# Optimization experiments

Hardware: AMD Instinct MI355X
Metric: run time of the kernel (lower is better)

Reference implementation:

```python
import jax, jax.numpy as jnp
import numpy as np
from jax import lax


def setup_inputs() -> dict:
    key = jax.random.key(0)
    k1, k2, k3, k4 = jax.random.split(key, 4)
    B, D, L = 2, 4096, 4096
    G, HL = 256, 128
    x = jax.random.normal(k1, (B, D, L), dtype=jnp.float32)
    k = jax.random.normal(k2, (B, D, L), dtype=jnp.float32)
    q = jax.random.normal(k3, (B, D, L), dtype=jnp.float32)
    h = jax.random.normal(k4, (G, HL), dtype=jnp.float32)
    return {"x": x, "k": k, "q": q, "h": h}


def reference(x, k, q, h):
    # Hyena-SE gated causal long conv (unfused_gcg reference path, bdl layout):
    #   kx = k * x ; y = causal_depthwise_conv(kx, h) ; out = q * y
    B, D, L = x.shape
    G, HL = h.shape
    # torch ref: h.squeeze(1).repeat(d // num_groups, 1)  -> tile filters over channels
    w = jnp.tile(h, (D // G, 1))[:, None, :]  # (D, 1, HL)
    kx = k * x
    y = lax.conv_general_dilated(
        kx, w,
        window_strides=(1,),
        padding=[(HL - 1, 0)],  # causal left pad
        dimension_numbers=("NCH", "OIH", "NCH"),
        feature_group_count=D,
    )  # (B, D, L)
    return q * y
```

## Files before the change

kernel.cpp:

```cpp
#include <hip/hip_runtime.h>


#define HSE_B  2
#define HSE_D  4096
#define HSE_L  4096
#define HSE_G  256
#define HSE_HL 128

constexpr int TPB  = 256;
constexpr int VPT  = 16;
constexpr int PAD  = 128;
constexpr int BUFN = PAD + HSE_L;
constexpr int ROWS = 4;
constexpr int GRID = (HSE_B * HSE_D) / ROWS;

__device__ __forceinline__ int swiz(int i) {
    return i ^ (((i >> 5) & 7) << 2);
}

__global__ __launch_bounds__(TPB, 4) void hyena_se_kernel(
    const float* __restrict__ x, const float* __restrict__ k,
    const float* __restrict__ q, const float* __restrict__ h,
    float* __restrict__ out)
{
    __shared__ float skx[2 * BUFN];

    const int tid  = threadIdx.x;
    const int t0   = tid * VPT;
    const int row0 = blockIdx.x * ROWS;

    if (tid < PAD / 4) {
        float4 z = make_float4(0.f, 0.f, 0.f, 0.f);
        ((float4*)skx)[swiz(4 * tid) >> 2] = z;
        ((float4*)(skx + BUFN))[swiz(4 * tid) >> 2] = z;
    }

    {
        const size_t row = (size_t)row0 * HSE_L;
        #pragma unroll
        for (int r = 0; r < HSE_L / (4 * TPB); ++r) {
            int pos = 4 * (tid + TPB * r);
            float4 xv = *(const float4*)(x + row + pos);
            float4 kv = *(const float4*)(k + row + pos);
            ((float4*)skx)[swiz(PAD + pos) >> 2] =
                make_float4(xv.x * kv.x, xv.y * kv.y, xv.z * kv.z, xv.w * kv.w);
        }
    }
    __syncthreads();

    for (int rr = 0; rr < ROWS; ++rr) {
        const int cur = rr & 1;
        float* __restrict__ buf = skx + cur * BUFN;
        const size_t row = (size_t)(row0 + rr) * HSE_L;
        const int d = (row0 + rr) & (HSE_D - 1);
        const float* __restrict__ hrow = h + (size_t)(d & (HSE_G - 1)) * HSE_HL;

        float4 qv[VPT / 4];
        #pragma unroll
        for (int m = 0; m < VPT / 4; ++m)
            qv[m] = *(const float4*)(q + row + t0 + 4 * m);

        float4 xn[4], kn[4];
        const bool more = (rr + 1 < ROWS);
        if (more) {
            const size_t nrow = row + HSE_L;
            #pragma unroll
            for (int r = 0; r < 4; ++r) {
                int pos = 4 * (tid + TPB * r);
                xn[r] = *(const float4*)(x + nrow + pos);
                kn[r] = *(const float4*)(k + nrow + pos);
            }
        }

        float acc[VPT];
        #pragma unroll
        for (int v = 0; v < VPT; ++v) acc[v] = 0.f;

        float w[24];
        #pragma unroll
        for (int m = 0; m < 4; ++m) {
            float4 wv = ((const float4*)buf)[swiz(t0 + 4 * m) >> 2];
            w[4*m+0] = wv.x; w[4*m+1] = wv.y; w[4*m+2] = wv.z; w[4*m+3] = wv.w;
        }

        #pragma unroll
        for (int jc = 0; jc < HSE_HL / 8; ++jc) {
            #pragma unroll
            for (int m = 0; m < 2; ++m) {
                float4 wv = ((const float4*)buf)[swiz(t0 + 8 * jc + 16 + 4 * m) >> 2];
                w[16 + 4*m + 0] = wv.x; w[16 + 4*m + 1] = wv.y;
                w[16 + 4*m + 2] = wv.z; w[16 + 4*m + 3] = wv.w;
            }
            float hf[8];
            #pragma unroll
            for (int u = 0; u < 8; ++u) hf[u] = hrow[8 * jc + u];

            #pragma unroll
            for (int v = 0; v < VPT; ++v) {
                #pragma unroll
                for (int u = 0; u < 8; ++u) {
                    acc[v] = fmaf(hf[u], w[1 + v + u], acc[v]);
                }
            }
            #pragma unroll
            for (int p = 0; p < 16; ++p) w[p] = w[p + 8];
        }

        #pragma unroll
        for (int m = 0; m < VPT / 4; ++m) {
            float4 o;
            o.x = qv[m].x * acc[4*m + 0];
            o.y = qv[m].y * acc[4*m + 1];
            o.z = qv[m].z * acc[4*m + 2];
            o.w = qv[m].w * acc[4*m + 3];
            *(float4*)(out + row + t0 + 4 * m) = o;
        }

        if (more) {
            float* __restrict__ nbuf = skx + (cur ^ 1) * BUFN;
            #pragma unroll
            for (int r = 0; r < 4; ++r) {
                int pos = 4 * (tid + TPB * r);
                ((float4*)nbuf)[swiz(PAD + pos) >> 2] = make_float4(
                    xn[r].x * kn[r].x, xn[r].y * kn[r].y,
                    xn[r].z * kn[r].z, xn[r].w * kn[r].w);
            }
        }
        __syncthreads();
    }
}

extern "C" void kernel_launch(void* const* d_in, const int* in_sizes, int n_in,
                              void* d_out, int out_size, void* d_ws, size_t ws_size,
                              hipStream_t stream) {
    const float* x = (const float*)d_in[0];
    const float* k = (const float*)d_in[1];
    const float* q = (const float*)d_in[2];
    const float* h = (const float*)d_in[3];
    float* o = (float*)d_out;

    dim3 grid(GRID);
    dim3 block(TPB);
    hyena_se_kernel<<<grid, block, 0, stream>>>(x, k, q, h, o);
}
```

Before: 460.9 us.

## Prefetch x/k via async global-to-LDS loads and use a persistent-style grid

```diff
diff --git a/kernel.cpp b/kernel.cpp
--- a/kernel.cpp
+++ b/kernel.cpp
@@ -10,67 +10,87 @@
 constexpr int TPB  = 256;
 constexpr int VPT  = 16;
 constexpr int PAD  = 128;
-constexpr int BUFN = PAD + HSE_L;
-constexpr int ROWS = 4;
-constexpr int GRID = (HSE_B * HSE_D) / ROWS;
+constexpr int LDS_KX = PAD + HSE_L;
+constexpr int GRID = 768;
+constexpr int BASE_ROWS = (HSE_B * HSE_D) / GRID;
 
 __device__ __forceinline__ int swiz(int i) {
     return i ^ (((i >> 5) & 7) << 2);
 }
 
-__global__ __launch_bounds__(TPB, 4) void hyena_se_kernel(
+__device__ __forceinline__ void gload16(const float* gp, float* lp) {
+    __builtin_amdgcn_global_load_lds(
+        (const __attribute__((address_space(1))) void*)gp,
+        (__attribute__((address_space(3))) void*)lp,
+        16, 0, 0);
+}
+
+__global__ __launch_bounds__(TPB, 3) void hyena_se_kernel(
     const float* __restrict__ x, const float* __restrict__ k,
     const float* __restrict__ q, const float* __restrict__ h,
     float* __restrict__ out)
 {
-    __shared__ float skx[2 * BUFN];
+    __shared__ __align__(16) float skx[LDS_KX];
+    __shared__ __align__(16) float sx[HSE_L];
+    __shared__ __align__(16) float sk[HSE_L];
 
-    const int tid  = threadIdx.x;
-    const int t0   = tid * VPT;
-    const int row0 = blockIdx.x * ROWS;
+    const int tid = threadIdx.x;
+    const int t0  = tid * VPT;
+    const int bid = blockIdx.x;
 
-    if (tid < PAD / 4) {
-        float4 z = make_float4(0.f, 0.f, 0.f, 0.f);
-        ((float4*)skx)[swiz(4 * tid) >> 2] = z;
-        ((float4*)(skx + BUFN))[swiz(4 * tid) >> 2] = z;
-    }
+    const int rem   = bid % 3;
+    const int nrows = BASE_ROWS + (rem != 2 ? 1 : 0);
+    const int row0  = BASE_ROWS * bid + 2 * (bid / 3) + (rem < 2 ? rem : 2);
+
+    if (tid < PAD / 4)
+        ((float4*)skx)[swiz(4 * tid) >> 2] = make_float4(0.f, 0.f, 0.f, 0.f);
 
     {
         const size_t row = (size_t)row0 * HSE_L;
         #pragma unroll
-        for (int r = 0; r < HSE_L / (4 * TPB); ++r) {
+        for (int r = 0; r < 4; ++r) {
             int pos = 4 * (tid + TPB * r);
-            float4 xv = *(const float4*)(x + row + pos);
-            float4 kv = *(const float4*)(k + row + pos);
+            gload16(x + row + pos, sx + pos);
+            gload16(k + row + pos, sk + pos);
+        }
+    }
+
+    for (int rr = 0; rr < nrows; ++rr) {
+        const size_t row = (size_t)(row0 + rr) * HSE_L;
+        const int d = (row0 + rr) & (HSE_D - 1);
+        const float* __restrict__ hrow = h + (size_t)(d & (HSE_G - 1)) * HSE_HL;
+
+        asm volatile("s_waitcnt vmcnt(0)" ::: "memory");
+
+        #pragma unroll
+        for (int r = 0; r < 4; ++r) {
+            int pos = 4 * (tid + TPB * r);
+            float4 xv = *(const float4*)(sx + pos);
+            float4 kv = *(const float4*)(sk + pos);
             ((float4*)skx)[swiz(PAD + pos) >> 2] =
                 make_float4(xv.x * kv.x, xv.y * kv.y, xv.z * kv.z, xv.w * kv.w);
         }
-    }
-    __syncthreads();
+        asm volatile("s_waitcnt lgkmcnt(0)" ::: "memory");
+        __builtin_amdgcn_sched_barrier(0);
 
-    for (int rr = 0; rr < ROWS; ++rr) {
-        const int cur = rr & 1;
-        float* __restrict__ buf = skx + cur * BUFN;
-        const size_t row = (size_t)(row0 + rr) * HSE_L;
-        const int d = (row0 + rr) & (HSE_D - 1);
-        const float* __restrict__ hrow = h + (size_t)(d & (HSE_G - 1)) * HSE_HL;
+        if (rr + 1 < nrows) {
+            const size_t nrow = row + HSE_L;
+            #pragma unroll
+            for (int r = 0; r < 4; ++r) {
+                int pos = 4 * (tid + TPB * r);
+                gload16(x + nrow + pos, sx + pos);
+                gload16(k + nrow + pos, sk + pos);
+            }
+        }
 
         float4 qv[VPT / 4];
         #pragma unroll
         for (int m = 0; m < VPT / 4; ++m)
             qv[m] = *(const float4*)(q + row + t0 + 4 * m);
 
-        float4 xn[4], kn[4];
-        const bool more = (rr + 1 < ROWS);
-        if (more) {
-            const size_t nrow = row + HSE_L;
-            #pragma unroll
-            for (int r = 0; r < 4; ++r) {
-                int pos = 4 * (tid + TPB * r);
-                xn[r] = *(const float4*)(x + nrow + pos);
-                kn[r] = *(const float4*)(k + nrow + pos);
-            }
-        }
+        __builtin_amdgcn_sched_barrier(0);
+        __builtin_amdgcn_s_barrier();
+        __builtin_amdgcn_sched_barrier(0);
 
         float acc[VPT];
         #pragma unroll
@@ -79,7 +99,7 @@
         float w[24];
         #pragma unroll
         for (int m = 0; m < 4; ++m) {
-            float4 wv = ((const float4*)buf)[swiz(t0 + 4 * m) >> 2];
+            float4 wv = ((const float4*)skx)[swiz(t0 + 4 * m) >> 2];
             w[4*m+0] = wv.x; w[4*m+1] = wv.y; w[4*m+2] = wv.z; w[4*m+3] = wv.w;
         }
 
@@ -87,7 +107,7 @@
         for (int jc = 0; jc < HSE_HL / 8; ++jc) {
             #pragma unroll
             for (int m = 0; m < 2; ++m) {
-                float4 wv = ((const float4*)buf)[swiz(t0 + 8 * jc + 16 + 4 * m) >> 2];
+                float4 wv = ((const float4*)skx)[swiz(t0 + 8 * jc + 16 + 4 * m) >> 2];
                 w[16 + 4*m + 0] = wv.x; w[16 + 4*m + 1] = wv.y;
                 w[16 + 4*m + 2] = wv.z; w[16 + 4*m + 3] = wv.w;
             }
@@ -116,17 +136,10 @@
             *(float4*)(out + row + t0 + 4 * m) = o;
         }
 
-        if (more) {
-            float* __restrict__ nbuf = skx + (cur ^ 1) * BUFN;
-            #pragma unroll
-            for (int r = 0; r < 4; ++r) {
-                int pos = 4 * (tid + TPB * r);
-                ((float4*)nbuf)[swiz(PAD + pos) >> 2] = make_float4(
-                    xn[r].x * kn[r].x, xn[r].y * kn[r].y,
-                    xn[r].z * kn[r].z, xn[r].w * kn[r].w);
-            }
-        }
-        __syncthreads();
+        asm volatile("s_waitcnt lgkmcnt(0)" ::: "memory");
+        __builtin_amdgcn_sched_barrier(0);
+        __builtin_amdgcn_s_barrier();
+        __builtin_amdgcn_sched_barrier(0);
     }
 }
 
```

Result: faster. 408.8 us (-11.3%).
